# Kernel tuning notes

Measured on AMD Instinct MI355X. Metric: run time of the kernel, lower is better.

## Reference

```python
import jax, jax.numpy as jnp
import numpy as np

B, S, D = 32, 512, 768
M, T = 32, 30
H, DFF, L, E = 12, 3072, 4, 100000
HD = D // H


def _layer_norm(x, w, b):
    m = jnp.mean(x, axis=-1, keepdims=True)
    v = jnp.var(x, axis=-1, keepdims=True)
    return (x - m) * jax.lax.rsqrt(v + 1e-5) * w + b


def _encoder_layer(x, p):
    # torch.nn.TransformerEncoderLayer, batch_first, post-LN, relu, eval (no dropout)
    wi, bi, wo, bo, g1, b1, w1, c1, w2, c2, g2, b2 = p
    qkv = x @ wi.T + bi                                   # [B,M,3D]
    q, k, v = jnp.split(qkv, 3, axis=-1)
    q = q.reshape(B, M, H, HD)
    k = k.reshape(B, M, H, HD)
    v = v.reshape(B, M, H, HD)
    a = jnp.einsum('bqhd,bkhd->bhqk', q, k) / np.float32(np.sqrt(HD))
    a = jax.nn.softmax(a, axis=-1)
    o = jnp.einsum('bhqk,bkhd->bqhd', a, v).reshape(B, M, D)
    x = _layer_norm(x + o @ wo.T + bo, g1, b1)
    ff = jax.nn.relu(x @ w1.T + c1) @ w2.T + c2
    return _layer_norm(x + ff, g2, b2)


def _forward(lhs, attn_w, attn_b, Wi, Bi, Wo, Bo, G1, B1, W1, C1, W2, C2, G2, B2v,
             cls_w1, cls_w2, cls_b2, pos, emask):
    # Vectorized form of the source triple loop: token slot x of mention (i,j) is
    # copied from last_hidden_state[i, x] while no -1 has been seen (break) and
    # the mention is active (entity_attention_mask != 0).
    valid = jnp.cumprod((pos != -1).astype(jnp.int32), axis=-1) > 0      # [B,M,T]
    valid = valid & (emask[:, :, None] != 0)
    mentions = jnp.where(valid[..., None], lhs[:, None, :T, :], 0.0)     # [B,M,T,D]
    scores = jax.nn.softmax(jnp.einsum('bmtd,d->bmt', mentions, attn_w) + attn_b, axis=-1)
    x = jnp.einsum('bmt,bmtd->bmd', scores, mentions)                    # attention pool
    for l in range(L):
        x = _encoder_layer(x, (Wi[l], Bi[l], Wo[l], Bo[l], G1[l], B1[l],
                               W1[l], C1[l], W2[l], C2[l], G2[l], B2v[l]))
    return (x @ cls_w1.T) @ cls_w2.T + cls_b2                            # [B,M,E]


def setup_inputs() -> dict:
    key = jax.random.key(0)
    k = jax.random.split(key, 12)
    lhs = jax.random.normal(k[0], (B, S, D), jnp.float32)
    pos = jax.random.randint(k[1], (B, M, T), 0, S)
    lens = jax.random.randint(k[2], (B, M), 0, T + 1)
    pos = jnp.where(jnp.arange(T)[None, None, :] < lens[..., None], pos, -1)
    emask = jax.random.randint(k[3], (B, M), 0, 2)
    s = 0.02
    return {
        'last_hidden_state': lhs,
        'attn_w': jax.random.normal(k[4], (D,), jnp.float32) * s,
        'attn_b': jnp.zeros((), jnp.float32),
        'in_proj_w': jax.random.normal(k[5], (L, 3 * D, D), jnp.float32) * s,
        'in_proj_b': jnp.zeros((L, 3 * D), jnp.float32),
        'out_w': jax.random.normal(k[6], (L, D, D), jnp.float32) * s,
        'out_b': jnp.zeros((L, D), jnp.float32),
        'ln1_w': jnp.ones((L, D), jnp.float32),
        'ln1_b': jnp.zeros((L, D), jnp.float32),
        'lin1_w': jax.random.normal(k[7], (L, DFF, D), jnp.float32) * s,
        'lin1_b': jnp.zeros((L, DFF), jnp.float32),
        'lin2_w': jax.random.normal(k[8], (L, D, DFF), jnp.float32) * s,
        'lin2_b': jnp.zeros((L, D), jnp.float32),
        'ln2_w': jnp.ones((L, D), jnp.float32),
        'ln2_b': jnp.zeros((L, D), jnp.float32),
        'cls_w1': jax.random.normal(k[9], (100, D), jnp.float32) * s,
        'cls_w2': jax.random.normal(k[10], (E, 100), jnp.float32) * s,
        'cls_b2': jnp.zeros((E,), jnp.float32),
        'entity_position_ids': pos,
        'entity_attention_mask': emask,
    }


def reference(last_hidden_state, attn_w, attn_b, in_proj_w, in_proj_b, out_w, out_b,
              ln1_w, ln1_b, lin1_w, lin1_b, lin2_w, lin2_b, ln2_w, ln2_b,
              cls_w1, cls_w2, cls_b2, entity_position_ids, entity_attention_mask):
    return _forward(last_hidden_state, attn_w, attn_b, in_proj_w, in_proj_b, out_w, out_b,
                    ln1_w, ln1_b, lin1_w, lin1_b, lin2_w, lin2_b, ln2_w, ln2_b,
                    cls_w1, cls_w2, cls_b2, entity_position_ids, entity_attention_mask)
```

## Files before the change

### kernel.cpp

```cpp
#include <hip/hip_runtime.h>

constexpr int Bc = 32, Sc = 512, Dc = 768, Mc = 32, Tc = 30;
constexpr int Hc = 12, DFFc = 3072, Lc = 4, Ec = 100000, HDc = 64;
constexpr int TOK = Bc * Mc;
constexpr int KC2 = 112;

typedef float floatx4 __attribute__((ext_vector_type(4)));
typedef __bf16 bfrag8 __attribute__((ext_vector_type(8)));
typedef unsigned short usx8 __attribute__((ext_vector_type(8)));
typedef unsigned short usx4 __attribute__((ext_vector_type(4)));

__device__ __forceinline__ unsigned short f32_to_bf16(float f) {
    unsigned int u = __float_as_uint(f);
    unsigned int r = (u + 0x7FFFu + ((u >> 16) & 1u)) >> 16;
    return (unsigned short)r;
}

struct CvtSegs {
    const float* src[7];
    unsigned short* dst[7];
    unsigned int end[7];
    unsigned int total;
};

__global__ __launch_bounds__(256)
void cvt_multi_kernel(CvtSegs a) {
    const unsigned int stride = gridDim.x * 256;
    for (unsigned int i = blockIdx.x * 256 + threadIdx.x; i < a.total; i += stride) {
        int s = 0;
        while (i >= a.end[s]) ++s;
        const unsigned int off = i - (s ? a.end[s - 1] : 0u);
        usx4 o = (usx4)0;
        if (a.src[s]) {
            floatx4 v = *(const floatx4*)(a.src[s] + 4 * (size_t)off);
            #pragma unroll
            for (int j = 0; j < 4; ++j) o[j] = f32_to_bf16(v[j]);
        }
        *(usx4*)(a.dst[s] + 4 * (size_t)off) = o;
    }
}

__global__ __launch_bounds__(256)
void cvt_c2_kernel(const float* __restrict__ src, unsigned short* __restrict__ dst) {
    const int total = Ec * (KC2 / 8);
    const int stride = gridDim.x * 256;
    for (int c = blockIdx.x * 256 + threadIdx.x; c < total; c += stride) {
        const int row = c / 14, j = c - 14 * (c / 14);
        const int col0 = j * 8;
        const float* sp = src + (size_t)row * 100 + col0;
        usx8 o = (usx8)0;
        if (col0 + 8 <= 100) {
            floatx4 v0 = *(const floatx4*)(sp);
            floatx4 v1 = *(const floatx4*)(sp + 4);
            #pragma unroll
            for (int jj = 0; jj < 4; ++jj) { o[jj] = f32_to_bf16(v0[jj]); o[4 + jj] = f32_to_bf16(v1[jj]); }
        } else {
            #pragma unroll
            for (int jj = 0; jj < 8; ++jj)
                if (col0 + jj < 100) o[jj] = f32_to_bf16(sp[jj]);
        }
        *(usx8*)(dst + (size_t)row * KC2 + col0) = o;
    }
}

__global__ __launch_bounds__(256)
void pool_kernel(const float* __restrict__ lhs, const float* __restrict__ attn_w,
                 const int* __restrict__ pos, const int* __restrict__ emask,
                 float* __restrict__ x0, unsigned short* __restrict__ x0b) {
    const int bm = blockIdx.x;
    const int b = bm >> 5;
    const int tid = threadIdx.x;
    __shared__ float s_logit[32];
    __shared__ float s_w[32];
    __shared__ int s_valid[32];

    if (tid == 0) {
        int em = emask[bm];
        int ok = 1;
        for (int t = 0; t < Tc; ++t) {
            if (pos[bm * Tc + t] == -1) ok = 0;
            s_valid[t] = (ok && em) ? 1 : 0;
        }
    }
    __syncthreads();

    const int wid = tid >> 6, lane = tid & 63;
    for (int t = wid; t < Tc; t += 4) {
        float p = 0.f;
        const float* row = lhs + ((size_t)b * Sc + t) * Dc;
        for (int d = lane; d < Dc; d += 64) p += row[d] * attn_w[d];
        #pragma unroll
        for (int off = 32; off > 0; off >>= 1) p += __shfl_down(p, off);
        if (lane == 0) s_logit[t] = s_valid[t] ? p : 0.0f;
    }
    __syncthreads();
    if (tid == 0) {
        float mx = -1e30f;
        for (int t = 0; t < Tc; ++t) mx = fmaxf(mx, s_logit[t]);
        float sum = 0.f;
        for (int t = 0; t < Tc; ++t) { float e = expf(s_logit[t] - mx); s_w[t] = e; sum += e; }
        float inv = 1.0f / sum;
        for (int t = 0; t < Tc; ++t) s_w[t] = s_valid[t] ? s_w[t] * inv : 0.0f;
    }
    __syncthreads();
    for (int d = tid; d < Dc; d += 256) {
        float acc = 0.f;
        for (int t = 0; t < Tc; ++t) acc += s_w[t] * lhs[((size_t)b * Sc + t) * Dc + d];
        x0[(size_t)bm * Dc + d] = acc;
        x0b[(size_t)bm * Dc + d] = f32_to_bf16(acc);
    }
}

template <int BM, int BN, int WM, int WN, int OUTBF>
__global__ __launch_bounds__(256)
void gemm_bf16_kernel(const unsigned short* __restrict__ A, int lda,
                      const unsigned short* __restrict__ B, int ldb,
                      const float* __restrict__ bias, void* __restrict__ Cv,
                      int ldc, int M, int N, int K, int relu, int nxReal) {
    constexpr int BK = 64;
    constexpr int LK = BK + 8;
    __shared__ unsigned short lA[BM * LK];
    __shared__ unsigned short lB[BN * LK];

    int bx, by;
    if (nxReal > 0) {
        const int gx = gridDim.x, gy = gridDim.y;
        const int lb = blockIdx.y * gx + blockIdx.x;
        const int xcd = lb & 7, p = lb >> 3;
        const int pq = p / gy;
        bx = xcd * (gx >> 3) + pq;
        by = p - pq * gy;
        if (bx >= nxReal) return;
    } else {
        bx = blockIdx.x; by = blockIdx.y;
    }
    const int z = blockIdx.z;
    A += (size_t)z * K;
    B += (size_t)z * K;

    const int tid = threadIdx.x;
    const int bm0 = by * BM;
    const int bn0 = bx * BN;

    const int wid = tid >> 6;
    const int lane = tid & 63;
    const int quad = lane >> 4;
    const int l16 = lane & 15;
    const int wr = (wid >> 1) * (WM * 16);
    const int wc = (wid & 1) * (WN * 16);

    const int tr = tid >> 3;
    const int tk = (tid & 7) * 8;

    floatx4 acc[WM][WN] = {};

    for (int k0 = 0; k0 < K; k0 += BK) {
        const int gk0 = k0 + tk;
        for (int r = tr; r < BM; r += 32) {
            const unsigned short* ap = A + (size_t)(bm0 + r) * lda + gk0;
            usx8 t8 = (usx8)0;
            if (gk0 + 8 <= K) {
                t8 = *(const usx8*)ap;
            } else {
                #pragma unroll
                for (int j = 0; j < 8; ++j)
                    if (gk0 + j < K) t8[j] = ap[j];
            }
            *(usx8*)(&lA[r * LK + tk]) = t8;
        }
        for (int r = tr; r < BN; r += 32) {
            const int gn = bn0 + r;
            usx8 t8 = (usx8)0;
            if (gn < N) {
                const unsigned short* bp = B + (size_t)gn * ldb + gk0;
                if (gk0 + 8 <= K) {
                    t8 = *(const usx8*)bp;
                } else {
                    #pragma unroll
                    for (int j = 0; j < 8; ++j)
                        if (gk0 + j < K) t8[j] = bp[j];
                }
            }
            *(usx8*)(&lB[r * LK + tk]) = t8;
        }
        __syncthreads();
        #pragma unroll
        for (int kk = 0; kk < BK; kk += 32) {
            bfrag8 af[WM], bfr[WN];
            #pragma unroll
            for (int i = 0; i < WM; ++i)
                af[i] = *(const bfrag8*)(&lA[(wr + i * 16 + l16) * LK + kk + quad * 8]);
            #pragma unroll
            for (int j = 0; j < WN; ++j)
                bfr[j] = *(const bfrag8*)(&lB[(wc + j * 16 + l16) * LK + kk + quad * 8]);
            #pragma unroll
            for (int i = 0; i < WM; ++i)
                #pragma unroll
                for (int j = 0; j < WN; ++j)
                    acc[i][j] = __builtin_amdgcn_mfma_f32_16x16x32_bf16(af[i], bfr[j], acc[i][j], 0, 0, 0);
        }
        __syncthreads();
    }

    #pragma unroll
    for (int i = 0; i < WM; ++i) {
        #pragma unroll
        for (int j = 0; j < WN; ++j) {
            const int col = bn0 + wc + j * 16 + l16;
            if (col < N) {
                const int row0 = bm0 + wr + i * 16 + quad * 4;
                const float bv = bias ? bias[col] : 0.0f;
                #pragma unroll
                for (int r = 0; r < 4; ++r) {
                    float v = acc[i][j][r] + bv;
                    if (relu) v = fmaxf(v, 0.0f);
                    const size_t idx = (size_t)z * M * ldc + (size_t)(row0 + r) * ldc + col;
                    if (OUTBF) ((unsigned short*)Cv)[idx] = f32_to_bf16(v);
                    else       ((float*)Cv)[idx] = v;
                }
            }
        }
    }
}

__global__ __launch_bounds__(256)
void attn_kernel(const float* __restrict__ qkv, unsigned short* __restrict__ outb) {
    const int bh = blockIdx.x;
    const int b = bh / Hc, h = bh % Hc;
    const int tid = threadIdx.x;
    __shared__ float sQ[32][65];
    __shared__ float sK[32][65];
    __shared__ float sV[32][65];
    __shared__ float sS[32][33];

    const int m = tid >> 3;
    const int c0 = (tid & 7) * 8;
    {
        const size_t rbase = ((size_t)(b * 32 + m)) * (3 * Dc);
        #pragma unroll
        for (int j = 0; j < 8; ++j) {
            sQ[m][c0 + j] = qkv[rbase + h * HDc + c0 + j];
            sK[m][c0 + j] = qkv[rbase + Dc + h * HDc + c0 + j];
            sV[m][c0 + j] = qkv[rbase + 2 * Dc + h * HDc + c0 + j];
        }
    }
    __syncthreads();

    #pragma unroll
    for (int u = 0; u < 4; ++u) {
        const int e = tid * 4 + u;
        const int q = e >> 5, k = e & 31;
        float s = 0.f;
        #pragma unroll
        for (int d = 0; d < HDc; ++d) s += sQ[q][d] * sK[k][d];
        sS[q][k] = s * 0.125f;
    }
    __syncthreads();
    if (tid < 32) {
        float mx = -1e30f;
        for (int k = 0; k < 32; ++k) mx = fmaxf(mx, sS[tid][k]);
        float sum = 0.f;
        for (int k = 0; k < 32; ++k) { float e = expf(sS[tid][k] - mx); sS[tid][k] = e; sum += e; }
        const float inv = 1.0f / sum;
        for (int k = 0; k < 32; ++k) sS[tid][k] *= inv;
    }
    __syncthreads();
    float o[8] = {};
    for (int k = 0; k < 32; ++k) {
        const float p = sS[m][k];
        #pragma unroll
        for (int j = 0; j < 8; ++j) o[j] += p * sV[k][c0 + j];
    }
    usx8 o8;
    #pragma unroll
    for (int j = 0; j < 8; ++j) o8[j] = f32_to_bf16(o[j]);
    *(usx8*)(&outb[((size_t)(b * 32 + m)) * Dc + h * HDc + c0]) = o8;
}

__global__ __launch_bounds__(256)
void addln_kernel(const float* __restrict__ xa, const float* __restrict__ xs, int nslab,
                  const float* __restrict__ badd, const float* __restrict__ g,
                  const float* __restrict__ be, float* __restrict__ outf,
                  unsigned short* __restrict__ outb) {
    const int row = blockIdx.x;
    const int tid = threadIdx.x;
    __shared__ float red[8];
    float v[3];
    float s = 0.f, sq = 0.f;
    #pragma unroll
    for (int i = 0; i < 3; ++i) {
        const int d = tid + i * 256;
        float x = xa[(size_t)row * Dc + d] + badd[d];
        for (int sl = 0; sl < nslab; ++sl)
            x += xs[((size_t)sl * TOK + row) * Dc + d];
        v[i] = x; s += x; sq += x * x;
    }
    #pragma unroll
    for (int off = 32; off > 0; off >>= 1) {
        s += __shfl_down(s, off);
        sq += __shfl_down(sq, off);
    }
    if ((tid & 63) == 0) { red[tid >> 6] = s; red[4 + (tid >> 6)] = sq; }
    __syncthreads();
    const float ts = red[0] + red[1] + red[2] + red[3];
    const float tq = red[4] + red[5] + red[6] + red[7];
    const float mean = ts * (1.0f / Dc);
    const float var = tq * (1.0f / Dc) - mean * mean;
    const float inv = rsqrtf(var + 1e-5f);
    #pragma unroll
    for (int i = 0; i < 3; ++i) {
        const int d = tid + i * 256;
        const float y = (v[i] - mean) * inv * g[d] + be[d];
        outf[(size_t)row * Dc + d] = y;
        outb[(size_t)row * Dc + d] = f32_to_bf16(y);
    }
}

extern "C" void kernel_launch(void* const* d_in, const int* in_sizes, int n_in,
                              void* d_out, int out_size, void* d_ws, size_t ws_size,
                              hipStream_t stream) {
    const float* lhs   = (const float*)d_in[0];
    const float* attnw = (const float*)d_in[1];
    const float* ipw = (const float*)d_in[3];
    const float* ipb = (const float*)d_in[4];
    const float* oww = (const float*)d_in[5];
    const float* owb = (const float*)d_in[6];
    const float* g1  = (const float*)d_in[7];
    const float* b1  = (const float*)d_in[8];
    const float* l1w = (const float*)d_in[9];
    const float* l1b = (const float*)d_in[10];
    const float* l2w = (const float*)d_in[11];
    const float* l2b = (const float*)d_in[12];
    const float* g2  = (const float*)d_in[13];
    const float* b2  = (const float*)d_in[14];
    const float* cw1 = (const float*)d_in[15];
    const float* cw2 = (const float*)d_in[16];
    const float* cb2 = (const float*)d_in[17];
    const int* pos   = (const int*)d_in[18];
    const int* emask = (const int*)d_in[19];
    float* out = (float*)d_out;

    constexpr size_t N_IP = (size_t)Lc * 3 * Dc * Dc;
    constexpr size_t N_OW = (size_t)Lc * Dc * Dc;
    constexpr size_t N_L1 = (size_t)Lc * DFFc * Dc;
    constexpr size_t N_L2 = (size_t)Lc * Dc * DFFc;
    constexpr size_t N_C1 = (size_t)KC2 * Dc;

    char* ws = (char*)d_ws;
    unsigned short* bw_c2 = (unsigned short*)ws;
    unsigned short* bufCb = bw_c2 + (size_t)Ec * KC2;

    constexpr size_t F_XA   = (size_t)TOK * Dc;
    constexpr size_t F_QKV  = (size_t)TOK * 3 * Dc;
    constexpr size_t F_SLAB = (size_t)4 * TOK * Dc;
    constexpr size_t S_ACT  = (size_t)TOK * Dc;
    constexpr size_t S_FFH  = (size_t)TOK * DFFc;
    constexpr size_t tail_bytes =
        4 * (F_XA + F_XA + F_QKV + F_SLAB) +
        2 * (N_IP + N_OW + N_L1 + N_L2 + N_C1 + 3 * S_ACT + S_FFH);

    const size_t out_bytes = (size_t)out_size * 4;
    char* tail = (char*)d_out + ((out_bytes - tail_bytes) & ~(size_t)255);

    float* xA   = (float*)tail;
    float* xB   = xA + F_XA;
    float* qkvb = xB + F_XA;
    float* bufS = qkvb + F_QKV;
    unsigned short* bw_ip = (unsigned short*)(bufS + F_SLAB);
    unsigned short* bw_ow = bw_ip + N_IP;
    unsigned short* bw_l1 = bw_ow + N_OW;
    unsigned short* bw_l2 = bw_l1 + N_L1;
    unsigned short* bw_c1 = bw_l2 + N_L2;
    unsigned short* xAb   = bw_c1 + N_C1;
    unsigned short* xBb   = xAb + S_ACT;
    unsigned short* attnb = xBb + S_ACT;
    unsigned short* bufHb = attnb + S_ACT;

    {
        CvtSegs segs{};
        const float* srcs[6] = {ipw, oww, l1w, l2w, cw1, nullptr};
        unsigned short* dsts[6] = {bw_ip, bw_ow, bw_l1, bw_l2, bw_c1, bw_c1 + (size_t)100 * Dc};
        const unsigned int cnt[6] = {(unsigned)(N_IP / 4), (unsigned)(N_OW / 4),
                                     (unsigned)(N_L1 / 4), (unsigned)(N_L2 / 4),
                                     (unsigned)(100 * Dc / 4), (unsigned)(12 * Dc / 4)};
        unsigned int acc = 0;
        for (int i = 0; i < 6; ++i) { segs.src[i] = srcs[i]; segs.dst[i] = dsts[i]; acc += cnt[i]; segs.end[i] = acc; }
        segs.src[6] = nullptr; segs.dst[6] = dsts[5]; segs.end[6] = 0xFFFFFFFFu;
        segs.total = acc;
        cvt_multi_kernel<<<2048, 256, 0, stream>>>(segs);
    }
    cvt_c2_kernel<<<1024, 256, 0, stream>>>(cw2, bw_c2);

    pool_kernel<<<TOK, 256, 0, stream>>>(lhs, attnw, pos, emask, xA, xAb);

    auto g64 = [&](const unsigned short* A, int lda, const unsigned short* B, int ldb,
                   const float* bias, void* C, int ldc, int N, int K, int relu,
                   int ks, int outbf, bool swz) {
        int gx = (N + 63) / 64, nx = -1;
        if (swz) { nx = gx; gx = (gx + 7) & ~7; }
        dim3 grid(gx, TOK / 64, ks);
        if (outbf) gemm_bf16_kernel<64, 64, 2, 2, 1><<<grid, 256, 0, stream>>>(A, lda, B, ldb, bias, C, ldc, TOK, N, K, relu, nx);
        else       gemm_bf16_kernel<64, 64, 2, 2, 0><<<grid, 256, 0, stream>>>(A, lda, B, ldb, bias, C, ldc, TOK, N, K, relu, nx);
    };

    for (int l = 0; l < Lc; ++l) {
        g64(xAb, Dc, bw_ip + (size_t)l * 3 * Dc * Dc, Dc, ipb + (size_t)l * 3 * Dc,
            qkvb, 3 * Dc, 3 * Dc, Dc, 0, 1, 0, false);
        attn_kernel<<<Bc * Hc, 256, 0, stream>>>(qkvb, attnb);
        g64(attnb, Dc, bw_ow + (size_t)l * Dc * Dc, Dc, nullptr,
            bufS, Dc, Dc, Dc / 4, 0, 4, 0, false);
        addln_kernel<<<TOK, 256, 0, stream>>>(xA, bufS, 4, owb + (size_t)l * Dc,
                                              g1 + (size_t)l * Dc, b1 + (size_t)l * Dc, xB, xBb);
        g64(xBb, Dc, bw_l1 + (size_t)l * DFFc * Dc, Dc, l1b + (size_t)l * DFFc,
            bufHb, DFFc, DFFc, Dc, 1, 1, 1, true);
        g64(bufHb, DFFc, bw_l2 + (size_t)l * Dc * DFFc, DFFc, nullptr,
            bufS, Dc, Dc, DFFc / 4, 0, 4, 0, false);
        addln_kernel<<<TOK, 256, 0, stream>>>(xB, bufS, 4, l2b + (size_t)l * Dc,
                                              g2 + (size_t)l * Dc, b2 + (size_t)l * Dc, xA, xAb);
    }

    g64(xAb, Dc, bw_c1, Dc, nullptr, bufCb, KC2, KC2, Dc, 0, 1, 1, false);
    {
        int nx = (Ec + 127) / 128;
        int gx = (nx + 7) & ~7;
        dim3 grid(gx, TOK / 128, 1);
        gemm_bf16_kernel<128, 128, 4, 4, 0><<<grid, 256, 0, stream>>>(
            bufCb, KC2, bw_c2, KC2, cb2, out, Ec, TOK, Ec, KC2, 0, nx);
    }
}
```

Before: 1.198 ms.

## Load GEMM tiles directly into LDS with XOR-swizzled layout

Replaces the register-staged global-to-LDS tile loads in the bf16 MFMA GEMM with direct global_load_lds 16-byte transfers, dropping the padded LDS rows in favour of an XOR swizzle to avoid bank conflicts. To remove the K and N tail bounds checks, the classifier K dimension is padded from 112 to 128 and the cls_w1 padding rows are extended to 28, so all tiles are full. This cuts VGPR traffic and per-element guards in the loader, but relies on every GEMM having K a multiple of 64 and N-padded buffers being readable.

```diff
diff --git a/kernel.cpp b/kernel.cpp
--- a/kernel.cpp
+++ b/kernel.cpp
@@ -3,7 +3,7 @@
 constexpr int Bc = 32, Sc = 512, Dc = 768, Mc = 32, Tc = 30;
 constexpr int Hc = 12, DFFc = 3072, Lc = 4, Ec = 100000, HDc = 64;
 constexpr int TOK = Bc * Mc;
-constexpr int KC2 = 112;
+constexpr int KC2 = 128;
 
 typedef float floatx4 __attribute__((ext_vector_type(4)));
 typedef __bf16 bfrag8 __attribute__((ext_vector_type(8)));
@@ -14,6 +14,10 @@
     unsigned int u = __float_as_uint(f);
     unsigned int r = (u + 0x7FFFu + ((u >> 16) & 1u)) >> 16;
     return (unsigned short)r;
+}
+
+__device__ __forceinline__ void gload_lds16(const void* gsrc, void* lds) {
+    __builtin_amdgcn_global_load_lds((const unsigned int*)gsrc, (unsigned int*)lds, 16, 0, 0);
 }
 
 struct CvtSegs {
@@ -45,7 +49,7 @@
     const int total = Ec * (KC2 / 8);
     const int stride = gridDim.x * 256;
     for (int c = blockIdx.x * 256 + threadIdx.x; c < total; c += stride) {
-        const int row = c / 14, j = c - 14 * (c / 14);
+        const int row = c >> 4, j = c & 15;
         const int col0 = j * 8;
         const float* sp = src + (size_t)row * 100 + col0;
         usx8 o = (usx8)0;
@@ -54,7 +58,7 @@
             floatx4 v1 = *(const floatx4*)(sp + 4);
             #pragma unroll
             for (int jj = 0; jj < 4; ++jj) { o[jj] = f32_to_bf16(v0[jj]); o[4 + jj] = f32_to_bf16(v1[jj]); }
-        } else {
+        } else if (col0 < 100) {
             #pragma unroll
             for (int jj = 0; jj < 8; ++jj)
                 if (col0 + jj < 100) o[jj] = f32_to_bf16(sp[jj]);
@@ -118,9 +122,8 @@
                       const float* __restrict__ bias, void* __restrict__ Cv,
                       int ldc, int M, int N, int K, int relu, int nxReal) {
     constexpr int BK = 64;
-    constexpr int LK = BK + 8;
-    __shared__ unsigned short lA[BM * LK];
-    __shared__ unsigned short lB[BN * LK];
+    __shared__ unsigned short lA[BM * BK];
+    __shared__ unsigned short lB[BN * BK];
 
     int bx, by;
     if (nxReal > 0) {
@@ -149,50 +152,43 @@
     const int wr = (wid >> 1) * (WM * 16);
     const int wc = (wid & 1) * (WN * 16);
 
-    const int tr = tid >> 3;
-    const int tk = (tid & 7) * 8;
-
     floatx4 acc[WM][WN] = {};
 
     for (int k0 = 0; k0 < K; k0 += BK) {
-        const int gk0 = k0 + tk;
-        for (int r = tr; r < BM; r += 32) {
-            const unsigned short* ap = A + (size_t)(bm0 + r) * lda + gk0;
-            usx8 t8 = (usx8)0;
-            if (gk0 + 8 <= K) {
-                t8 = *(const usx8*)ap;
-            } else {
-                #pragma unroll
-                for (int j = 0; j < 8; ++j)
-                    if (gk0 + j < K) t8[j] = ap[j];
-            }
-            *(usx8*)(&lA[r * LK + tk]) = t8;
-        }
-        for (int r = tr; r < BN; r += 32) {
-            const int gn = bn0 + r;
-            usx8 t8 = (usx8)0;
-            if (gn < N) {
-                const unsigned short* bp = B + (size_t)gn * ldb + gk0;
-                if (gk0 + 8 <= K) {
-                    t8 = *(const usx8*)bp;
-                } else {
-                    #pragma unroll
-                    for (int j = 0; j < 8; ++j)
-                        if (gk0 + j < K) t8[j] = bp[j];
-                }
-            }
-            *(usx8*)(&lB[r * LK + tk]) = t8;
+        #pragma unroll
+        for (int it = 0; it < BM / 32; ++it) {
+            const int chunk = wid * (BM / 32) + it;
+            const int boff = chunk * 1024 + lane * 16;
+            const int row = boff >> 7;
+            const int cb = (boff & 127) ^ ((row & 7) << 4);
+            gload_lds16((const char*)(A + (size_t)(bm0 + row) * lda + k0) + cb,
+                        &lA[chunk * 512]);
+        }
+        #pragma unroll
+        for (int it = 0; it < BN / 32; ++it) {
+            const int chunk = wid * (BN / 32) + it;
+            const int boff = chunk * 1024 + lane * 16;
+            const int row = boff >> 7;
+            const int cb = (boff & 127) ^ ((row & 7) << 4);
+            gload_lds16((const char*)(B + (size_t)(bn0 + row) * ldb + k0) + cb,
+                        &lB[chunk * 512]);
         }
         __syncthreads();
         #pragma unroll
         for (int kk = 0; kk < BK; kk += 32) {
             bfrag8 af[WM], bfr[WN];
             #pragma unroll
-            for (int i = 0; i < WM; ++i)
-                af[i] = *(const bfrag8*)(&lA[(wr + i * 16 + l16) * LK + kk + quad * 8]);
-            #pragma unroll
-            for (int j = 0; j < WN; ++j)
-                bfr[j] = *(const bfrag8*)(&lB[(wc + j * 16 + l16) * LK + kk + quad * 8]);
+            for (int i = 0; i < WM; ++i) {
+                const int rowA = wr + i * 16 + l16;
+                af[i] = *(const bfrag8*)((const char*)lA + rowA * 128 +
+                                         ((kk * 2 + quad * 16) ^ ((rowA & 7) << 4)));
+            }
+            #pragma unroll
+            for (int j = 0; j < WN; ++j) {
+                const int rowB = wc + j * 16 + l16;
+                bfr[j] = *(const bfrag8*)((const char*)lB + rowB * 128 +
+                                          ((kk * 2 + quad * 16) ^ ((rowB & 7) << 4)));
+            }
             #pragma unroll
             for (int i = 0; i < WM; ++i)
                 #pragma unroll
@@ -382,7 +378,7 @@
         unsigned short* dsts[6] = {bw_ip, bw_ow, bw_l1, bw_l2, bw_c1, bw_c1 + (size_t)100 * Dc};
         const unsigned int cnt[6] = {(unsigned)(N_IP / 4), (unsigned)(N_OW / 4),
                                      (unsigned)(N_L1 / 4), (unsigned)(N_L2 / 4),
-                                     (unsigned)(100 * Dc / 4), (unsigned)(12 * Dc / 4)};
+                                     (unsigned)(100 * Dc / 4), (unsigned)(28 * Dc / 4)};
         unsigned int acc = 0;
         for (int i = 0; i < 6; ++i) { segs.src[i] = srcs[i]; segs.dst[i] = dsts[i]; acc += cnt[i]; segs.end[i] = acc; }
         segs.src[6] = nullptr; segs.dst[6] = dsts[5]; segs.end[6] = 0xFFFFFFFFu;
```

New measurement: 1.000 ms. 16.5% less time.
